# Kernel optimization log

Hardware: AMD Instinct MI355X
Metric: run time of the kernel (lower is better)

Reference implementation:

```python
import jax, jax.numpy as jnp
import numpy as np

K = 4
TEMPERATURE = 30.0


def setup_inputs() -> dict:
    key = jax.random.key(0)
    ks = jax.random.split(key, 6)
    B, C, H, W_sp = 32, 128, 56, 56
    Cout, kh, kw = 128, 3, 3
    Cred = max(C // 4, 1)
    x = jax.random.normal(ks[0], (B, C, H, W_sp), dtype=jnp.float32)
    # K parallel conv kernels + biases (fan-in scaled init)
    fan = C * kh * kw
    W = jax.random.normal(ks[1], (K, Cout, C, kh, kw), dtype=jnp.float32) / np.sqrt(fan)
    b = jax.random.normal(ks[2], (K, Cout), dtype=jnp.float32) * 0.01
    # attention branch: 1x1 convs == dense on pooled features
    aw1 = jax.random.normal(ks[3], (Cred, C), dtype=jnp.float32) / np.sqrt(C)
    aw2 = jax.random.normal(ks[4], (K, Cred), dtype=jnp.float32) / np.sqrt(Cred)
    return {"x": x, "W": W, "b": b, "aw1": aw1, "aw2": aw2}


def reference(x, W, b, aw1, aw2):
    # attention: global avg pool -> 1x1 conv (dense) -> relu -> 1x1 conv -> softmax(logits/T)
    pooled = jnp.mean(x, axis=(2, 3))                       # [B, C]
    h1 = jax.nn.relu(jnp.einsum('bc,rc->br', pooled, aw1))  # [B, Cred]
    logits = jnp.einsum('br,kr->bk', h1, aw2)               # [B, K]
    attn = jax.nn.softmax(logits / TEMPERATURE, axis=1)     # [B, K]

    pad = 1
    out = None
    for i in range(K):  # fixed small K, structurally distinct kernels
        yi = jax.lax.conv_general_dilated(
            x, W[i], window_strides=(1, 1), padding=[(pad, pad), (pad, pad)],
            dimension_numbers=('NCHW', 'OIHW', 'NCHW'))
        yi = yi + b[i][None, :, None, None]
        yi = yi * attn[:, i][:, None, None, None]
        out = yi if out is None else out + yi
    return out
```

## Files before the change

### kernel.cpp

```cpp
#include <hip/hip_runtime.h>
#include <hip/hip_bf16.h>
#include <stdint.h>

typedef __bf16 bf16x8 __attribute__((ext_vector_type(8)));
typedef float  f32x4  __attribute__((ext_vector_type(4)));
typedef unsigned short u16x8 __attribute__((ext_vector_type(8)));

#define NB 32
#define NC 128
#define NH 56
#define NW 56
#define NK 4
#define NCO 128
#define NCR 32
#define NHW 3136
#define TEMPER 30.0f

#define WS_ATTN   0u
#define WS_BC     4096u
#define WS_ROWSUM 65536u
#define WS_WC     1048576u
#define WS_XT     10485760u

__global__ void xt_kernel(const float* __restrict__ x, __hip_bfloat16* __restrict__ xt,
                          float* __restrict__ rowsum) {
  __shared__ float lds[58 * 133];
  int xcd = blockIdx.x & 7;
  int j   = blockIdx.x >> 3;
  int b   = xcd * 4 + j / 58;
  int hp  = j % 58;
  int blk = b * 58 + hp;
  int h = hp - 1;
  bool hin = (h >= 0) && (h < NH);
  int tid = threadIdx.x;
  if (hin) {
    const float* xrow = x + ((size_t)b * NC) * NHW + (size_t)h * NW;
    for (int i = tid; i < 128 * 14; i += 256) {
      int c = i / 14;
      int w4 = (i - c * 14) * 4;
      float4 v = *(const float4*)(xrow + (size_t)c * NHW + w4);
      int base = (w4 + 1) * 133 + c;
      lds[base]         = v.x;
      lds[base + 133]   = v.y;
      lds[base + 2*133] = v.z;
      lds[base + 3*133] = v.w;
    }
  }
  __syncthreads();
  __hip_bfloat16* orow = xt + (size_t)blk * (58 * 128);
  for (int i = tid; i < 58 * 16; i += 256) {
    int wp = i >> 4;
    int cg = (i & 15) << 3;
    u16x8 o;
    if (!hin || wp == 0 || wp == 57) {
      o = (u16x8)0;
    } else {
      const float* src = lds + wp * 133 + cg;
      #pragma unroll
      for (int jx = 0; jx < 8; ++jx) {
        union { __hip_bfloat16 b; unsigned short u; } cv;
        cv.b = __float2bfloat16(src[jx]);
        o[jx] = cv.u;
      }
    }
    *(u16x8*)(orow + wp * 128 + cg) = o;
  }
  if (hin && tid < 128) {
    float s = 0.f;
    #pragma unroll 8
    for (int wp = 1; wp <= 56; ++wp) s += lds[wp * 133 + tid];
    rowsum[(size_t)blk * 128 + tid] = s;
  }
}

__global__ void attn_kernel(const float* __restrict__ rowsum, const float* __restrict__ aw1,
                            const float* __restrict__ aw2, const float* __restrict__ bias,
                            float* __restrict__ attn, float* __restrict__ bc_out) {
  int b = blockIdx.x;
  __shared__ float sp[NC], h1[NCR], at[NK];
  int t = threadIdx.x;
  if (t < NC) {
    float s = 0.f;
    for (int hp = 1; hp <= 56; ++hp) s += rowsum[((size_t)b * 58 + hp) * 128 + t];
    sp[t] = s * (1.0f / (float)NHW);
  }
  __syncthreads();
  if (t < NCR) {
    float s = 0.f;
    for (int c = 0; c < NC; ++c) s += aw1[t*NC + c] * sp[c];
    h1[t] = s > 0.f ? s : 0.f;
  }
  __syncthreads();
  if (t == 0) {
    float lg[NK], mx = -1e30f;
    for (int k = 0; k < NK; ++k) {
      float s = 0.f;
      for (int r = 0; r < NCR; ++r) s += aw2[k*NCR + r] * h1[r];
      lg[k] = s * (1.0f/TEMPER);
      mx = fmaxf(mx, lg[k]);
    }
    float den = 0.f, e[NK];
    for (int k = 0; k < NK; ++k) { e[k] = expf(lg[k]-mx); den += e[k]; }
    float inv = 1.0f/den;
    for (int k = 0; k < NK; ++k) { at[k] = e[k]*inv; attn[b*NK+k] = at[k]; }
  }
  __syncthreads();
  if (t < NCO) {
    float s = 0.f;
    for (int k = 0; k < NK; ++k) s += at[k] * bias[k*NCO + t];
    bc_out[b*NCO + t] = s;
  }
}

__global__ void combine_kernel(const float* __restrict__ W, const float* __restrict__ attn,
                               __hip_bfloat16* __restrict__ wc) {
  int gid = blockIdx.x;
  int bg  = gid >> 6;
  int tcell = (gid & 63) * 256 + threadIdx.x;
  int co = tcell >> 7, ci = tcell & 127;
  float w[4][9];
  const float* wp = W + ((size_t)co * 128 + ci) * 9;
  #pragma unroll
  for (int k = 0; k < 4; ++k)
    #pragma unroll
    for (int j = 0; j < 9; ++j)
      w[k][j] = wp[(size_t)k * 147456 + j];
  for (int b = bg * 8; b < bg * 8 + 8; ++b) {
    float a0 = attn[b*4+0], a1 = attn[b*4+1], a2 = attn[b*4+2], a3 = attn[b*4+3];
    #pragma unroll
    for (int j = 0; j < 9; ++j) {
      float v = a0*w[0][j] + a1*w[1][j] + a2*w[2][j] + a3*w[3][j];
      wc[(((size_t)b*9 + j) * 128 + co) * 128 + ci] = __float2bfloat16(v);
    }
  }
}

#define RS 2368
#define CS 40
#define BUFSH (6*RS)

#define GLOAD16(src, dst) \
  __builtin_amdgcn_global_load_lds( \
    (const __attribute__((address_space(1))) unsigned int*)(src), \
    (__attribute__((address_space(3))) unsigned int*)(dst), 16, 0, 0)

__global__ __launch_bounds__(256, 2) void conv_kernel(
    const unsigned short* __restrict__ xt,
    const unsigned short* __restrict__ wc,
    const float* __restrict__ bc,
    float* __restrict__ out) {
  __shared__ __align__(16) unsigned short lds_x[2*BUFSH];
  const int tid  = threadIdx.x;
  const int lane = tid & 63;
  const int wv   = tid >> 6;
  const int wave_m = wv & 1;
  const int wave_n = wv >> 1;
  const int bid = blockIdx.x;
  const int xcd = bid & 7;
  const int jj  = bid >> 3;
  const int b   = xcd * 4 + (jj / 14);
  const int r0  = (jj % 14) * 4;
  const int li = lane & 15;
  const int kg = lane >> 4;

  int srcoff[7];
  #pragma unroll
  for (int i = 0; i < 7; ++i) {
    int q = i*256 + tid;
    int r = q / 296;
    int sl = q - r*296;
    int col = sl / 5;
    int part = sl - col*5;
    if (q < 1776 && col < 58 && part < 4)
      srcoff[i] = ((r0 + r)*58 + col)*128 + part*8;
    else
      srcoff[i] = -1;
  }

  int rB[7], cB[7], xoff[7];
  #pragma unroll
  for (int f = 0; f < 7; ++f) {
    int pos = wave_n*112 + f*16 + li;
    rB[f] = pos / 56;
    cB[f] = pos - rB[f]*56;
    xoff[f] = rB[f]*RS + cB[f]*CS + kg*8;
  }
  const f32x4 vzero = {0.f, 0.f, 0.f, 0.f};
  f32x4 acc[4][7];
  #pragma unroll
  for (int mo = 0; mo < 4; ++mo)
    #pragma unroll
    for (int f = 0; f < 7; ++f) acc[mo][f] = vzero;

  const unsigned short* xtg = xt + (size_t)b*(58*58*128);
  const unsigned short* wcA = wc + (size_t)b*(9*128*128) + (wave_m*64 + li)*128 + kg*8;

  #define STAGE(bufidx, cc) do { \
    unsigned short* dbase = lds_x + (bufidx)*BUFSH; \
    _Pragma("unroll") \
    for (int i = 0; i < 7; ++i) { \
      if (srcoff[i] >= 0) \
        GLOAD16(xtg + srcoff[i] + (cc)*32, dbase + i*2048 + wv*512); \
    } \
  } while (0)

  #define LOADA(dst, cc, khw) do { \
    _Pragma("unroll") \
    for (int mo = 0; mo < 4; ++mo) \
      dst[mo] = *(const bf16x8*)(wcA + (khw)*16384 + mo*2048 + (cc)*32); \
  } while (0)

  bf16x8 afc[4], afn[4];
  LOADA(afc, 0, 0);
  STAGE(0, 0);
  __syncthreads();

  for (int cc = 0; cc < 4; ++cc) {
    if (cc < 3) STAGE((cc + 1) & 1, cc + 1);
    const unsigned short* bx = lds_x + (cc & 1)*BUFSH;
    #pragma unroll
    for (int khw = 0; khw < 9; ++khw) {
      if (khw < 8)      LOADA(afn, cc, khw + 1);
      else if (cc < 3)  LOADA(afn, cc + 1, 0);
      const int kh = khw / 3;
      const int kw = khw - kh*3;
      const int koff = kh*RS + kw*CS;
      bf16x8 bfr[7];
      #pragma unroll
      for (int f = 0; f < 7; ++f)
        bfr[f] = *(const bf16x8*)(bx + xoff[f] + koff);
      #pragma unroll
      for (int mo = 0; mo < 4; ++mo)
        #pragma unroll
        for (int f = 0; f < 7; ++f)
          acc[mo][f] = __builtin_amdgcn_mfma_f32_16x16x32_bf16(afc[mo], bfr[f], acc[mo][f], 0, 0, 0);
      #pragma unroll
      for (int mo = 0; mo < 4; ++mo) afc[mo] = afn[mo];
    }
    __syncthreads();
  }

  float* ob = out + (size_t)b*NCO*NHW;
  #pragma unroll
  for (int mo = 0; mo < 4; ++mo) {
    #pragma unroll
    for (int rg = 0; rg < 4; ++rg) {
      const int co = wave_m*64 + mo*16 + kg*4 + rg;
      const float bv = bc[b*NCO + co];
      float* orow = ob + (size_t)co*NHW;
      #pragma unroll
      for (int f = 0; f < 7; ++f)
        orow[(r0 + rB[f])*56 + cB[f]] = acc[mo][f][rg] + bv;
    }
  }
}

extern "C" void kernel_launch(void* const* d_in, const int* in_sizes, int n_in,
                              void* d_out, int out_size, void* d_ws, size_t ws_size,
                              hipStream_t stream) {
  const float* x   = (const float*)d_in[0];
  const float* W   = (const float*)d_in[1];
  const float* bia = (const float*)d_in[2];
  const float* aw1 = (const float*)d_in[3];
  const float* aw2 = (const float*)d_in[4];
  float* out = (float*)d_out;
  char* ws = (char*)d_ws;
  float* attn   = (float*)(ws + WS_ATTN);
  float* bcm    = (float*)(ws + WS_BC);
  float* rowsum = (float*)(ws + WS_ROWSUM);
  __hip_bfloat16* wc = (__hip_bfloat16*)(ws + WS_WC);
  __hip_bfloat16* xt = (__hip_bfloat16*)(ws + WS_XT);

  xt_kernel<<<NB*58, 256, 0, stream>>>(x, xt, rowsum);
  attn_kernel<<<NB, 128, 0, stream>>>(rowsum, aw1, aw2, bia, attn, bcm);
  combine_kernel<<<256, 256, 0, stream>>>(W, attn, wc);
  conv_kernel<<<448, 256, 0, stream>>>((const unsigned short*)xt,
                                       (const unsigned short*)wc, bcm, out);
}
```

Measured before the change: 76.54 us.

## Halve conv tile to two output rows, raise occupancy, drop A prefetch

```diff
diff --git a/kernel.cpp b/kernel.cpp
--- a/kernel.cpp
+++ b/kernel.cpp
@@ -137,120 +137,116 @@
 
 #define RS 2368
 #define CS 40
-#define BUFSH (6*RS)
+#define BUF4 (4*RS)
 
 #define GLOAD16(src, dst) \
   __builtin_amdgcn_global_load_lds( \
     (const __attribute__((address_space(1))) unsigned int*)(src), \
     (__attribute__((address_space(3))) unsigned int*)(dst), 16, 0, 0)
 
-__global__ __launch_bounds__(256, 2) void conv_kernel(
+__global__ __launch_bounds__(256, 4) void conv_kernel(
     const unsigned short* __restrict__ xt,
     const unsigned short* __restrict__ wc,
     const float* __restrict__ bc,
     float* __restrict__ out) {
-  __shared__ __align__(16) unsigned short lds_x[2*BUFSH];
+  __shared__ __align__(16) unsigned short lds_x[2*BUF4];
   const int tid  = threadIdx.x;
   const int lane = tid & 63;
   const int wv   = tid >> 6;
-  const int wave_m = wv & 1;
-  const int wave_n = wv >> 1;
   const int bid = blockIdx.x;
   const int xcd = bid & 7;
   const int jj  = bid >> 3;
-  const int b   = xcd * 4 + (jj / 14);
-  const int r0  = (jj % 14) * 4;
+  const int b   = xcd * 4 + (jj / 28);
+  const int r0  = (jj % 28) * 2;
   const int li = lane & 15;
   const int kg = lane >> 4;
 
-  int srcoff[7];
-  #pragma unroll
-  for (int i = 0; i < 7; ++i) {
+  int srcoff[5];
+  #pragma unroll
+  for (int i = 0; i < 5; ++i) {
     int q = i*256 + tid;
     int r = q / 296;
     int sl = q - r*296;
     int col = sl / 5;
     int part = sl - col*5;
-    if (q < 1776 && col < 58 && part < 4)
+    if (q < 1184 && col < 58 && part < 4)
       srcoff[i] = ((r0 + r)*58 + col)*128 + part*8;
     else
       srcoff[i] = -1;
   }
 
-  int rB[7], cB[7], xoff[7];
+  int xoff[7];
   #pragma unroll
   for (int f = 0; f < 7; ++f) {
-    int pos = wave_n*112 + f*16 + li;
-    rB[f] = pos / 56;
-    cB[f] = pos - rB[f]*56;
-    xoff[f] = rB[f]*RS + cB[f]*CS + kg*8;
+    int pos = f*16 + li;
+    int rB = pos / 56;
+    int cB = pos - rB*56;
+    xoff[f] = rB*RS + cB*CS + kg*8;
   }
   const f32x4 vzero = {0.f, 0.f, 0.f, 0.f};
-  f32x4 acc[4][7];
-  #pragma unroll
-  for (int mo = 0; mo < 4; ++mo)
+  f32x4 acc[2][7];
+  #pragma unroll
+  for (int mo = 0; mo < 2; ++mo)
     #pragma unroll
     for (int f = 0; f < 7; ++f) acc[mo][f] = vzero;
 
   const unsigned short* xtg = xt + (size_t)b*(58*58*128);
-  const unsigned short* wcA = wc + (size_t)b*(9*128*128) + (wave_m*64 + li)*128 + kg*8;
+  const unsigned short* wcA = wc + (size_t)b*(9*128*128) + (wv*32 + li)*128 + kg*8;
 
   #define STAGE(bufidx, cc) do { \
-    unsigned short* dbase = lds_x + (bufidx)*BUFSH; \
+    unsigned short* dbase = lds_x + (bufidx)*BUF4; \
     _Pragma("unroll") \
-    for (int i = 0; i < 7; ++i) { \
+    for (int i = 0; i < 5; ++i) { \
       if (srcoff[i] >= 0) \
         GLOAD16(xtg + srcoff[i] + (cc)*32, dbase + i*2048 + wv*512); \
     } \
   } while (0)
 
-  #define LOADA(dst, cc, khw) do { \
-    _Pragma("unroll") \
-    for (int mo = 0; mo < 4; ++mo) \
-      dst[mo] = *(const bf16x8*)(wcA + (khw)*16384 + mo*2048 + (cc)*32); \
-  } while (0)
-
-  bf16x8 afc[4], afn[4];
-  LOADA(afc, 0, 0);
   STAGE(0, 0);
   __syncthreads();
 
   for (int cc = 0; cc < 4; ++cc) {
     if (cc < 3) STAGE((cc + 1) & 1, cc + 1);
-    const unsigned short* bx = lds_x + (cc & 1)*BUFSH;
+    const unsigned short* bx = lds_x + (cc & 1)*BUF4;
     #pragma unroll
     for (int khw = 0; khw < 9; ++khw) {
-      if (khw < 8)      LOADA(afn, cc, khw + 1);
-      else if (cc < 3)  LOADA(afn, cc + 1, 0);
       const int kh = khw / 3;
       const int kw = khw - kh*3;
       const int koff = kh*RS + kw*CS;
+      bf16x8 af[2];
+      #pragma unroll
+      for (int mo = 0; mo < 2; ++mo)
+        af[mo] = *(const bf16x8*)(wcA + khw*16384 + mo*2048 + cc*32);
       bf16x8 bfr[7];
       #pragma unroll
       for (int f = 0; f < 7; ++f)
         bfr[f] = *(const bf16x8*)(bx + xoff[f] + koff);
-      #pragma unroll
-      for (int mo = 0; mo < 4; ++mo)
+      __builtin_amdgcn_s_setprio(1);
+      #pragma unroll
+      for (int mo = 0; mo < 2; ++mo)
         #pragma unroll
         for (int f = 0; f < 7; ++f)
-          acc[mo][f] = __builtin_amdgcn_mfma_f32_16x16x32_bf16(afc[mo], bfr[f], acc[mo][f], 0, 0, 0);
-      #pragma unroll
-      for (int mo = 0; mo < 4; ++mo) afc[mo] = afn[mo];
+          acc[mo][f] = __builtin_amdgcn_mfma_f32_16x16x32_bf16(af[mo], bfr[f], acc[mo][f], 0, 0, 0);
+      __builtin_amdgcn_s_setprio(0);
     }
     __syncthreads();
   }
 
   float* ob = out + (size_t)b*NCO*NHW;
   #pragma unroll
-  for (int mo = 0; mo < 4; ++mo) {
+  for (int mo = 0; mo < 2; ++mo) {
     #pragma unroll
     for (int rg = 0; rg < 4; ++rg) {
-      const int co = wave_m*64 + mo*16 + kg*4 + rg;
+      const int co = wv*32 + mo*16 + kg*4 + rg;
       const float bv = bc[b*NCO + co];
       float* orow = ob + (size_t)co*NHW;
       #pragma unroll
-      for (int f = 0; f < 7; ++f)
-        orow[(r0 + rB[f])*56 + cB[f]] = acc[mo][f][rg] + bv;
+      for (int f = 0; f < 7; ++f) {
+        int pos = f*16 + li;
+        int rB = pos / 56;
+        int cB = pos - rB*56;
+        orow[(r0 + rB)*56 + cB] = acc[mo][f][rg] + bv;
+      }
     }
   }
 }
@@ -274,6 +270,6 @@
   xt_kernel<<<NB*58, 256, 0, stream>>>(x, xt, rowsum);
   attn_kernel<<<NB, 128, 0, stream>>>(rowsum, aw1, aw2, bia, attn, bcm);
   combine_kernel<<<256, 256, 0, stream>>>(W, attn, wc);
-  conv_kernel<<<448, 256, 0, stream>>>((const unsigned short*)xt,
+  conv_kernel<<<896, 256, 0, stream>>>((const unsigned short*)xt,
                                        (const unsigned short*)wc, bcm, out);
 }
```

After: 77.19 us. About the same (+0.8%).
